# Kernel tuning notes

Hardware: AMD Instinct MI355X
Metric: run time of the kernel (lower is better)

Reference implementation:

```python
import jax, jax.numpy as jnp
import numpy as np
from jax import lax

B, T, D, H = 2048, 512, 8, 80  # batch, seq_len, input_dim, hidden_dim


def setup_inputs() -> dict:
    key = jax.random.key(0)
    ks = jax.random.split(key, 10)
    s = 1.0 / np.sqrt(H)  # torch LSTM init: U(-1/sqrt(H), 1/sqrt(H))
    u = lambda k, shape: jax.random.uniform(k, shape, jnp.float32, -s, s)
    return {
        "X": jax.random.normal(ks[0], (B, T, D), jnp.float32),
        "W_ih0": u(ks[1], (4 * H, D)),
        "W_hh0": u(ks[2], (4 * H, H)),
        "b_ih0": u(ks[3], (4 * H,)),
        "b_hh0": u(ks[4], (4 * H,)),
        "W_ih1": u(ks[5], (4 * H, H)),
        "W_hh1": u(ks[6], (4 * H, H)),
        "b_ih1": u(ks[7], (4 * H,)),
        "b_hh1": u(ks[8], (4 * H,)),
        "X_seq_len": jax.random.randint(ks[9], (B,), 1, T + 1),  # valid lengths in [1, T]
    }


def _lstm_layer(x_tm, W_ih, W_hh, b_ih, b_hh):
    """x_tm: [T, B, Din] time-major. Returns hidden states [T, B, H].
    PyTorch gate order: i, f, g, o."""
    # Precompute all input projections in one big GEMM: [T, B, 4H]
    xg = jnp.einsum('tbd,gd->tbg', x_tm, W_ih) + b_ih + b_hh
    Hd = W_hh.shape[1]
    h0 = jnp.zeros((x_tm.shape[1], Hd), x_tm.dtype)

    def step(carry, g_in):
        h, c = carry
        g = g_in + h @ W_hh.T  # [B, 4H]
        i, f, gg, o = jnp.split(g, 4, axis=-1)
        c = jax.nn.sigmoid(f) * c + jax.nn.sigmoid(i) * jnp.tanh(gg)
        h = jax.nn.sigmoid(o) * jnp.tanh(c)
        return (h, c), h

    _, hs = lax.scan(step, (h0, h0), xg)
    return hs


def reference(X, W_ih0, W_hh0, b_ih0, b_hh0, W_ih1, W_hh1, b_ih1, b_hh1, X_seq_len):
    x = jnp.swapaxes(X, 0, 1)  # [T, B, D] time-major for scan
    h1 = _lstm_layer(x, W_ih0, W_hh0, b_ih0, b_hh0)   # [T, B, H]
    h2 = _lstm_layer(h1, W_ih1, W_hh1, b_ih1, b_hh1)  # [T, B, H]
    # Gather last valid timestep per sequence (packed-seq semantics):
    # state at t = len-1 only depends on inputs <= len-1, so padded run is equivalent.
    idx = X_seq_len - 1
    out = h2[idx, jnp.arange(X.shape[0])]  # [B, H]
    return out
```

## Files before the change

### kernel.cpp

```cpp
#include <hip/hip_runtime.h>
#include <math.h>

#define B_   2048
#define T_   512
#define D_   8
#define H_   80
#define NB   16
#define NBLK (B_ / NB)
#define NTH  640
#define KS0  3
#define KS1  5
#define A0S  256
#define A1S  384
#define A0BUF (16 * A0S)
#define A1BUF (16 * A1S)
#define LOG2E 1.44269504f
#define K2    2.88539008f

typedef float f32x4  __attribute__((ext_vector_type(4)));
typedef short bf16x8 __attribute__((ext_vector_type(8)));
typedef unsigned short u16x4 __attribute__((ext_vector_type(4)));

__device__ __forceinline__ float E2(float x) {
#if __has_builtin(__builtin_amdgcn_exp2f)
  return __builtin_amdgcn_exp2f(x);
#else
  return __expf(x * 0.6931471806f);
#endif
}
__device__ __forceinline__ unsigned short f2bf(float f) {
  unsigned u = __builtin_bit_cast(unsigned, f);
  return (unsigned short)((u + 0x7FFFu + ((u >> 16) & 1u)) >> 16);
}
__device__ __forceinline__ float bf2f(unsigned short b) {
  unsigned u = ((unsigned)b) << 16;
  return __builtin_bit_cast(float, u);
}
__device__ __forceinline__ int swz(int row, int byte_in_row) {
  return byte_in_row ^ ((row & 7) << 4);
}
__device__ __forceinline__ float cell(float ai, float af, float ag, float ao,
                                      float& c) {
  const float ei = E2(-ai), ef = E2(-af), eg = E2(-ag), eo = E2(-ao);
  const float P  = (1.0f + ei) * (1.0f + eg);
  const float pf = 1.0f + ef;
  const float cn = __builtin_fmaf(c, P, (1.0f - eg) * pf)
                 * __builtin_amdgcn_rcpf(P * pf);
  c = cn;
  const float ec = E2(-K2 * fabsf(cn));
  const float t  = (1.0f - ec)
                 * __builtin_amdgcn_rcpf((1.0f + eo) * (1.0f + ec));
  return copysignf(t, cn);
}

__global__ __launch_bounds__(512)
void sort_by_len(const int* __restrict__ slen, int* __restrict__ perm) {
  __shared__ int cnt[513];
  const int tid = threadIdx.x;
  for (int i = tid; i < 513; i += 512) cnt[i] = 0;
  __syncthreads();
  for (int b = tid; b < B_; b += 512) atomicAdd(&cnt[T_ - slen[b]], 1);
  __syncthreads();
  if (tid == 0) { int s = 0;
    for (int k = 0; k < 513; ++k) { int c = cnt[k]; cnt[k] = s; s += c; } }
  __syncthreads();
  for (int b = tid; b < B_; b += 512) {
    int pos = atomicAdd(&cnt[T_ - slen[b]], 1);
    perm[pos] = b;
  }
}

__global__ __launch_bounds__(NTH)
void lstm2_mfma(const float* __restrict__ X,
                const float* __restrict__ Wih0, const float* __restrict__ Whh0,
                const float* __restrict__ bih0, const float* __restrict__ bhh0,
                const float* __restrict__ Wih1, const float* __restrict__ Whh1,
                const float* __restrict__ bih1, const float* __restrict__ bhh1,
                const int* __restrict__ slen, const int* __restrict__ perm,
                float* __restrict__ out)
{
  __shared__ char a0lds[2 * A0BUF];
  __shared__ char a1lds[2 * A1BUF];
  __shared__ int  pbs[NB];
  __shared__ int  lns[NB];

  const int tid = threadIdx.x;
  const int w   = tid >> 6;
  const int l   = tid & 63;
  const int lr  = l & 15;
  const int q   = l >> 4;
  const int L   = (w < 5) ? 0 : 1;
  const int v   = w - 5 * L;
  const int u   = 16 * v + lr;
  const int ub4 = 16 * v + 4 * q;

  if (tid < NB) {
    int pb = perm[blockIdx.x * NB + tid];
    pbs[tid] = pb;
    lns[tid] = slen[pb];
  }

  bf16x8 wf[4][KS1];
  float  bias[4][4];
  if (L == 0) {
    #pragma unroll
    for (int g = 0; g < 4; ++g) {
      const float sc = (g == 2) ? K2 : LOG2E;
      const int n = 80 * g + u;
      #pragma unroll
      for (int r = 0; r < 4; ++r) {
        const int nb = 80 * g + ub4 + r;
        bias[g][r] = (bih0[nb] + bhh0[nb]) * sc;
      }
      #pragma unroll
      for (int ks = 0; ks < KS0; ++ks) {
        bf16x8 vv;
        #pragma unroll
        for (int j = 0; j < 8; ++j) {
          int k = 32 * ks + 8 * q + j;
          float f = (k < 8)  ? Wih0[n * D_ + k]
                  : (k < 16) ? Wih0[n * D_ + (k - 8)]
                             : Whh0[n * H_ + (k - 16)];
          vv[j] = (short)f2bf(f * sc);
        }
        wf[g][ks] = vv;
      }
    }
  } else {
    #pragma unroll
    for (int g = 0; g < 4; ++g) {
      const float sc = (g == 2) ? K2 : LOG2E;
      const int n = 80 * g + u;
      #pragma unroll
      for (int r = 0; r < 4; ++r) {
        const int nb = 80 * g + ub4 + r;
        bias[g][r] = (bih1[nb] + bhh1[nb]) * sc;
      }
      #pragma unroll
      for (int ks = 0; ks < KS1; ++ks) {
        bf16x8 vv;
        #pragma unroll
        for (int j = 0; j < 8; ++j) {
          int k = 32 * ks + 8 * q + j;
          float f = (k < 80) ? Wih1[n * H_ + k] : Whh1[n * H_ + (k - 80)];
          vv[j] = (short)f2bf(f * sc);
        }
        wf[g][ks] = vv;
      }
    }
  }

  for (int i = tid; i < (2 * A0BUF) / 4; i += NTH) ((int*)a0lds)[i] = 0;
  for (int i = tid; i < (2 * A1BUF) / 4; i += NTH) ((int*)a1lds)[i] = 0;
  __syncthreads();

  const int mlen  = lns[0];
  const int pbseq = pbs[lr];
  const int lm1   = lns[lr] - 1;

  const int xs = tid >> 4, xt = (tid & 15) >> 1, xh = tid & 1;
  const float* xbase = nullptr;
  f32x4 xa = {}, xb = {};
  if (tid < 256) {
    xbase = X + (size_t)pbs[xs] * (T_ * D_) + 4 * xh;
    int t0 = xt;     if (t0 > T_ - 1) t0 = T_ - 1;
    int t1 = 8 + xt; if (t1 > T_ - 1) t1 = T_ - 1;
    xa = *(const f32x4*)(xbase + t0 * D_);
    xb = *(const f32x4*)(xbase + t1 * D_);
  }
  #pragma unroll
  for (int tt = 0; tt < 2; ++tt) {
    if (tid < 256 && xt == tt) {
      u16x4 hi, lo;
      #pragma unroll
      for (int j = 0; j < 4; ++j) { hi[j] = f2bf(xa[j]); lo[j] = f2bf(xa[j] - bf2f(hi[j])); }
      char* buf = a0lds + tt * A0BUF;
      *(u16x4*)(buf + xs * A0S + swz(xs, 8 * xh))      = hi;
      *(u16x4*)(buf + xs * A0S + swz(xs, 16 + 8 * xh)) = lo;
    }
  }
  __syncthreads();

  float c[4] = {0.f, 0.f, 0.f, 0.f};

  if (L == 0) {
    f32x4 acc[4] = {};
    #pragma unroll
    for (int ks = 0; ks < KS0; ++ks) {
      bf16x8 a = *(const bf16x8*)(a0lds + lr * A0S + swz(lr, 64 * ks + 16 * q));
      #pragma unroll
      for (int g = 0; g < 4; ++g)
        acc[g] = __builtin_amdgcn_mfma_f32_16x16x32_bf16(wf[g][ks], a, acc[g], 0, 0, 0);
    }
    char* A1w = a1lds;
    char* A0w = a0lds + A0BUF;
    u16x4 hv;
    #pragma unroll
    for (int r = 0; r < 4; ++r) {
      float h = cell(acc[0][r] + bias[0][r], acc[1][r] + bias[1][r],
                     acc[2][r] + bias[2][r], acc[3][r] + bias[3][r], c[r]);
      hv[r] = f2bf(h);
    }
    *(u16x4*)(A1w + lr * A1S + swz(lr, 2 * ub4))      = hv;
    *(u16x4*)(A0w + lr * A0S + swz(lr, 32 + 2 * ub4)) = hv;
  }
  __syncthreads();

  #pragma unroll 2
  for (int i = 0; i < mlen; ++i) {
    const int cur = i & 1, nxt = cur ^ 1;

    if (tid < 256 && ((i + 2) & 7) == 0) {
      xa = xb;
      int tc = i + 10 + xt; if (tc > T_ - 1) tc = T_ - 1;
      xb = *(const f32x4*)(xbase + tc * D_);
    }

    f32x4 acc[4] = {};
    if (L == 1) {
      const char* A1p = a1lds + cur * A1BUF;
      #pragma unroll
      for (int ks = 0; ks < KS1; ++ks) {
        bf16x8 a = *(const bf16x8*)(A1p + lr * A1S + swz(lr, 64 * ks + 16 * q));
        #pragma unroll
        for (int g = 0; g < 4; ++g)
          acc[g] = __builtin_amdgcn_mfma_f32_16x16x32_bf16(wf[g][ks], a, acc[g], 0, 0, 0);
      }
    } else {
      const char* A0p = a0lds + nxt * A0BUF;
      #pragma unroll
      for (int ks = 0; ks < KS0; ++ks) {
        bf16x8 a = *(const bf16x8*)(A0p + lr * A0S + swz(lr, 64 * ks + 16 * q));
        #pragma unroll
        for (int g = 0; g < 4; ++g)
          acc[g] = __builtin_amdgcn_mfma_f32_16x16x32_bf16(wf[g][ks], a, acc[g], 0, 0, 0);
      }
    }

    if (tid < 256 && xt == ((i + 2) & 7)) {
      u16x4 hi, lo;
      #pragma unroll
      for (int j = 0; j < 4; ++j) { hi[j] = f2bf(xa[j]); lo[j] = f2bf(xa[j] - bf2f(hi[j])); }
      char* buf = a0lds + cur * A0BUF;
      *(u16x4*)(buf + xs * A0S + swz(xs, 8 * xh))      = hi;
      *(u16x4*)(buf + xs * A0S + swz(xs, 16 + 8 * xh)) = lo;
    }

    char* A1n = a1lds + nxt * A1BUF;
    char* A0c = a0lds + cur * A0BUF;

    if (L == 1) {
      float h[4];
      u16x4 hv;
      #pragma unroll
      for (int r = 0; r < 4; ++r) {
        h[r] = cell(acc[0][r] + bias[0][r], acc[1][r] + bias[1][r],
                    acc[2][r] + bias[2][r], acc[3][r] + bias[3][r], c[r]);
        hv[r] = f2bf(h[r]);
      }
      *(u16x4*)(A1n + lr * A1S + swz(lr, 160 + 2 * ub4)) = hv;
      if (i == lm1)
        *(f32x4*)(out + (size_t)pbseq * H_ + ub4) = (f32x4){h[0], h[1], h[2], h[3]};
    } else {
      u16x4 hv;
      #pragma unroll
      for (int r = 0; r < 4; ++r) {
        float h = cell(acc[0][r] + bias[0][r], acc[1][r] + bias[1][r],
                       acc[2][r] + bias[2][r], acc[3][r] + bias[3][r], c[r]);
        hv[r] = f2bf(h);
      }
      *(u16x4*)(A1n + lr * A1S + swz(lr, 2 * ub4))      = hv;
      *(u16x4*)(A0c + lr * A0S + swz(lr, 32 + 2 * ub4)) = hv;
    }
    __syncthreads();
  }
}

extern "C" void kernel_launch(void* const* d_in, const int* in_sizes, int n_in,
                              void* d_out, int out_size, void* d_ws, size_t ws_size,
                              hipStream_t stream) {
  const float* X    = (const float*)d_in[0];
  const float* Wih0 = (const float*)d_in[1];
  const float* Whh0 = (const float*)d_in[2];
  const float* bih0 = (const float*)d_in[3];
  const float* bhh0 = (const float*)d_in[4];
  const float* Wih1 = (const float*)d_in[5];
  const float* Whh1 = (const float*)d_in[6];
  const float* bih1 = (const float*)d_in[7];
  const float* bhh1 = (const float*)d_in[8];
  const int*   slen = (const int*)d_in[9];
  int* perm = (int*)d_ws;

  sort_by_len<<<1, 512, 0, stream>>>(slen, perm);
  lstm2_mfma<<<NBLK, NTH, 0, stream>>>(
      X, Wih0, Whh0, bih0, bhh0, Wih1, Whh1, bih1, bhh1, slen, perm,
      (float*)d_out);
}
```

Measured before the change: 598.7 us.

## Split LSTM layers into producer/consumer blocks linked by a global-memory ring

Layer 0 and layer 1 of each 16-sequence group now run in two separate 320-thread blocks instead of one 640-thread block. Layer 0 publishes its hidden states into a 16-slot global ring buffer and a progress flag. Layer 1 spins on that flag and prefetches the next step's input from the ring, so each block syncs only its own five waves per step and the two layers can drift up to eight steps apart. The cost is global-memory traffic and atomic polling between blocks, and the scheme deadlocks unless both blocks of a pair are resident at the same time.

New measurement: 1.165 ms. 1.95x slower.

```diff
diff --git a/kernel.cpp b/kernel.cpp
--- a/kernel.cpp
+++ b/kernel.cpp
@@ -6,20 +6,23 @@
 #define D_   8
 #define H_   80
 #define NB   16
-#define NBLK (B_ / NB)
-#define NTH  640
+#define NPAIR (B_ / NB)
+#define NTH  320
 #define KS0  3
 #define KS1  5
 #define A0S  256
 #define A1S  384
 #define A0BUF (16 * A0S)
 #define A1BUF (16 * A1S)
+#define RING_D 16
+#define RSLOT  2560
 #define LOG2E 1.44269504f
 #define K2    2.88539008f
 
 typedef float f32x4  __attribute__((ext_vector_type(4)));
 typedef short bf16x8 __attribute__((ext_vector_type(8)));
 typedef unsigned short u16x4 __attribute__((ext_vector_type(4)));
+typedef unsigned long long u64;
 
 __device__ __forceinline__ float E2(float x) {
 #if __has_builtin(__builtin_amdgcn_exp2f)
@@ -54,9 +57,11 @@
 }
 
 __global__ __launch_bounds__(512)
-void sort_by_len(const int* __restrict__ slen, int* __restrict__ perm) {
+void sort_by_len(const int* __restrict__ slen, int* __restrict__ perm,
+                 int* __restrict__ flags) {
   __shared__ int cnt[513];
   const int tid = threadIdx.x;
+  if (tid < 256) flags[tid] = 0;
   for (int i = tid; i < 513; i += 512) cnt[i] = 0;
   __syncthreads();
   for (int b = tid; b < B_; b += 512) atomicAdd(&cnt[T_ - slen[b]], 1);
@@ -71,38 +76,41 @@
 }
 
 __global__ __launch_bounds__(NTH)
-void lstm2_mfma(const float* __restrict__ X,
-                const float* __restrict__ Wih0, const float* __restrict__ Whh0,
-                const float* __restrict__ bih0, const float* __restrict__ bhh0,
-                const float* __restrict__ Wih1, const float* __restrict__ Whh1,
-                const float* __restrict__ bih1, const float* __restrict__ bhh1,
-                const int* __restrict__ slen, const int* __restrict__ perm,
-                float* __restrict__ out)
+void lstm2_pc(const float* __restrict__ X,
+              const float* __restrict__ Wih0, const float* __restrict__ Whh0,
+              const float* __restrict__ bih0, const float* __restrict__ bhh0,
+              const float* __restrict__ Wih1, const float* __restrict__ Whh1,
+              const float* __restrict__ bih1, const float* __restrict__ bhh1,
+              const int* __restrict__ slen, const int* __restrict__ perm,
+              int* __restrict__ prog0, int* __restrict__ prog1,
+              char* __restrict__ ring, float* __restrict__ out)
 {
-  __shared__ char a0lds[2 * A0BUF];
-  __shared__ char a1lds[2 * A1BUF];
-  __shared__ int  pbs[NB];
-  __shared__ int  lns[NB];
+  __shared__ char lds[2 * A1BUF];
+  __shared__ int  pbs[NB], lns[NB];
 
   const int tid = threadIdx.x;
   const int w   = tid >> 6;
   const int l   = tid & 63;
   const int lr  = l & 15;
   const int q   = l >> 4;
-  const int L   = (w < 5) ? 0 : 1;
-  const int v   = w - 5 * L;
-  const int u   = 16 * v + lr;
-  const int ub4 = 16 * v + 4 * q;
+  const int u   = 16 * w + lr;
+  const int ub4 = 16 * w + 4 * q;
+  const int p   = blockIdx.x >> 1;
+  const int role = blockIdx.x & 1;
+
+  int* prog0p = prog0 + p;
+  int* prog1p = prog1 + p;
+  char* ringp = ring + (size_t)p * (RING_D * RSLOT);
 
   if (tid < NB) {
-    int pb = perm[blockIdx.x * NB + tid];
+    int pb = perm[p * NB + tid];
     pbs[tid] = pb;
     lns[tid] = slen[pb];
   }
 
-  bf16x8 wf[4][KS1];
-  float  bias[4][4];
-  if (L == 0) {
+  if (role == 0) {
+    bf16x8 wf[4][KS0];
+    float  bias[4][4];
     #pragma unroll
     for (int g = 0; g < 4; ++g) {
       const float sc = (g == 2) ? K2 : LOG2E;
@@ -126,7 +134,92 @@
         wf[g][ks] = vv;
       }
     }
+    for (int i = tid; i < (2 * A0BUF) / 4; i += NTH) ((int*)lds)[i] = 0;
+    __syncthreads();
+    const int mlen = lns[0];
+
+    const int xs = tid >> 4, xt = (tid & 15) >> 1, xh = tid & 1;
+    const float* xbase = nullptr;
+    f32x4 xa = {}, xb = {};
+    if (tid < 256) {
+      xbase = X + (size_t)pbs[xs] * (T_ * D_) + 4 * xh;
+      int t0 = xt;     if (t0 > T_ - 1) t0 = T_ - 1;
+      int t1 = 8 + xt; if (t1 > T_ - 1) t1 = T_ - 1;
+      xa = *(const f32x4*)(xbase + t0 * D_);
+      xb = *(const f32x4*)(xbase + t1 * D_);
+    }
+    if (tid < 256 && xt == 0) {
+      u16x4 hi, lo;
+      #pragma unroll
+      for (int j = 0; j < 4; ++j) { hi[j] = f2bf(xa[j]); lo[j] = f2bf(xa[j] - bf2f(hi[j])); }
+      *(u16x4*)(lds + xs * A0S + swz(xs, 8 * xh))      = hi;
+      *(u16x4*)(lds + xs * A0S + swz(xs, 16 + 8 * xh)) = lo;
+    }
+    __syncthreads();
+
+    float c[4] = {0.f, 0.f, 0.f, 0.f};
+    int p1c = 0;
+
+    #pragma unroll 2
+    for (int i = 0; i < mlen; ++i) {
+      if (tid == 0)
+        __hip_atomic_store(prog0p, i, __ATOMIC_RELEASE, __HIP_MEMORY_SCOPE_AGENT);
+      if ((i & 7) == 0 && i >= 16) {
+        const int target = i - 8;
+        if (p1c < target) {
+          int pv;
+          do {
+            pv = __hip_atomic_load(prog1p, __ATOMIC_ACQUIRE, __HIP_MEMORY_SCOPE_AGENT);
+            if (pv < target) __builtin_amdgcn_s_sleep(4);
+          } while (pv < target);
+          p1c = pv;
+        }
+      }
+      if (tid < 256 && ((i + 1) & 7) == 0) {
+        xa = xb;
+        int tc = i + 9 + xt; if (tc > T_ - 1) tc = T_ - 1;
+        xb = *(const f32x4*)(xbase + tc * D_);
+      }
+
+      const char* A0p = lds + (i & 1) * A0BUF;
+      f32x4 acc[4] = {};
+      #pragma unroll
+      for (int ks = 0; ks < KS0; ++ks) {
+        bf16x8 a = *(const bf16x8*)(A0p + lr * A0S + swz(lr, 64 * ks + 16 * q));
+        #pragma unroll
+        for (int g = 0; g < 4; ++g)
+          acc[g] = __builtin_amdgcn_mfma_f32_16x16x32_bf16(wf[g][ks], a, acc[g], 0, 0, 0);
+      }
+
+      char* A0n = lds + ((i + 1) & 1) * A0BUF;
+      if (tid < 256 && xt == ((i + 1) & 7)) {
+        u16x4 hi, lo;
+        #pragma unroll
+        for (int j = 0; j < 4; ++j) { hi[j] = f2bf(xa[j]); lo[j] = f2bf(xa[j] - bf2f(hi[j])); }
+        *(u16x4*)(A0n + xs * A0S + swz(xs, 8 * xh))      = hi;
+        *(u16x4*)(A0n + xs * A0S + swz(xs, 16 + 8 * xh)) = lo;
+      }
+
+      u16x4 hv;
+      #pragma unroll
+      for (int r = 0; r < 4; ++r) {
+        float h = cell(acc[0][r] + bias[0][r], acc[1][r] + bias[1][r],
+                       acc[2][r] + bias[2][r], acc[3][r] + bias[3][r], c[r]);
+        hv[r] = f2bf(h);
+      }
+      *(u16x4*)(A0n + lr * A0S + swz(lr, 32 + 2 * ub4)) = hv;
+      __hip_atomic_store((u64*)(ringp + (size_t)(i & (RING_D - 1)) * RSLOT
+                                + lr * 160 + 2 * ub4),
+                         __builtin_bit_cast(u64, hv),
+                         __ATOMIC_RELAXED, __HIP_MEMORY_SCOPE_AGENT);
+      __syncthreads();
+    }
+    if (tid == 0)
+      __hip_atomic_store(prog0p, mlen, __ATOMIC_RELEASE, __HIP_MEMORY_SCOPE_AGENT);
+
   } else {
+    bf16x8 wf[4][KS1];
+    float  bias[4][4];
     #pragma unroll
     for (int g = 0; g < 4; ++g) {
       const float sc = (g == 2) ? K2 : LOG2E;
@@ -148,77 +241,56 @@
         wf[g][ks] = vv;
       }
     }
-  }
-
-  for (int i = tid; i < (2 * A0BUF) / 4; i += NTH) ((int*)a0lds)[i] = 0;
-  for (int i = tid; i < (2 * A1BUF) / 4; i += NTH) ((int*)a1lds)[i] = 0;
-  __syncthreads();
-
-  const int mlen  = lns[0];
-  const int pbseq = pbs[lr];
-  const int lm1   = lns[lr] - 1;
-
-  const int xs = tid >> 4, xt = (tid & 15) >> 1, xh = tid & 1;
-  const float* xbase = nullptr;
-  f32x4 xa = {}, xb = {};
-  if (tid < 256) {
-    xbase = X + (size_t)pbs[xs] * (T_ * D_) + 4 * xh;
-    int t0 = xt;     if (t0 > T_ - 1) t0 = T_ - 1;
-    int t1 = 8 + xt; if (t1 > T_ - 1) t1 = T_ - 1;
-    xa = *(const f32x4*)(xbase + t0 * D_);
-    xb = *(const f32x4*)(xbase + t1 * D_);
-  }
-  #pragma unroll
-  for (int tt = 0; tt < 2; ++tt) {
-    if (tid < 256 && xt == tt) {
-      u16x4 hi, lo;
-      #pragma unroll
-      for (int j = 0; j < 4; ++j) { hi[j] = f2bf(xa[j]); lo[j] = f2bf(xa[j] - bf2f(hi[j])); }
-      char* buf = a0lds + tt * A0BUF;
-      *(u16x4*)(buf + xs * A0S + swz(xs, 8 * xh))      = hi;
-      *(u16x4*)(buf + xs * A0S + swz(xs, 16 + 8 * xh)) = lo;
-    }
-  }
-  __syncthreads();
-
-  float c[4] = {0.f, 0.f, 0.f, 0.f};
-
-  if (L == 0) {
-    f32x4 acc[4] = {};
-    #pragma unroll
-    for (int ks = 0; ks < KS0; ++ks) {
-      bf16x8 a = *(const bf16x8*)(a0lds + lr * A0S + swz(lr, 64 * ks + 16 * q));
-      #pragma unroll
-      for (int g = 0; g < 4; ++g)
-        acc[g] = __builtin_amdgcn_mfma_f32_16x16x32_bf16(wf[g][ks], a, acc[g], 0, 0, 0);
-    }
-    char* A1w = a1lds;
-    char* A0w = a0lds + A0BUF;
-    u16x4 hv;
-    #pragma unroll
-    for (int r = 0; r < 4; ++r) {
-      float h = cell(acc[0][r] + bias[0][r], acc[1][r] + bias[1][r],
-                     acc[2][r] + bias[2][r], acc[3][r] + bias[3][r], c[r]);
-      hv[r] = f2bf(h);
-    }
-    *(u16x4*)(A1w + lr * A1S + swz(lr, 2 * ub4))      = hv;
-    *(u16x4*)(A0w + lr * A0S + swz(lr, 32 + 2 * ub4)) = hv;
-  }
-  __syncthreads();
-
-  #pragma unroll 2
-  for (int i = 0; i < mlen; ++i) {
-    const int cur = i & 1, nxt = cur ^ 1;
-
-    if (tid < 256 && ((i + 2) & 7) == 0) {
-      xa = xb;
-      int tc = i + 10 + xt; if (tc > T_ - 1) tc = T_ - 1;
-      xb = *(const f32x4*)(xbase + tc * D_);
-    }
-
-    f32x4 acc[4] = {};
-    if (L == 1) {
-      const char* A1p = a1lds + cur * A1BUF;
+    for (int i = tid; i < (2 * A1BUF) / 4; i += NTH) ((int*)lds)[i] = 0;
+    __syncthreads();
+    const int mlen  = lns[0];
+    const int pbseq = pbs[lr];
+    const int lm1   = lns[lr] - 1;
+
+    const int ss = tid / 20, qd = tid - (tid / 20) * 20;
+    int p0c = 0;
+    {
+      const int target = (mlen < 5) ? mlen : 5;
+      int pv;
+      do {
+        pv = __hip_atomic_load(prog0p, __ATOMIC_ACQUIRE, __HIP_MEMORY_SCOPE_AGENT);
+        if (pv < target) __builtin_amdgcn_s_sleep(4);
+      } while (pv < target);
+      p0c = pv;
+    }
+    {
+      u64 v0 = __hip_atomic_load((const u64*)(ringp + ss * 160 + qd * 8),
+                                 __ATOMIC_RELAXED, __HIP_MEMORY_SCOPE_AGENT);
+      *(u64*)(lds + ss * A1S + swz(ss, qd * 8)) = v0;
+    }
+    __syncthreads();
+
+    float c[4] = {0.f, 0.f, 0.f, 0.f};
+
+    #pragma unroll 2
+    for (int i = 0; i < mlen; ++i) {
+      if ((i & 3) == 0) {
+        if (tid == 0)
+          __hip_atomic_store(prog1p, i, __ATOMIC_RELAXED, __HIP_MEMORY_SCOPE_AGENT);
+        int target = i + 5; if (target > mlen) target = mlen;
+        if (p0c < target) {
+          int pv;
+          do {
+            pv = __hip_atomic_load(prog0p, __ATOMIC_ACQUIRE, __HIP_MEMORY_SCOPE_AGENT);
+            if (pv < target) __builtin_amdgcn_s_sleep(4);
+          } while (pv < target);
+          p0c = pv;
+        }
+      }
+      const bool pf = (i + 1 < mlen);
+      u64 vst = 0;
+      if (pf)
+        vst = __hip_atomic_load((const u64*)(ringp
+                + (size_t)((i + 1) & (RING_D - 1)) * RSLOT + ss * 160 + qd * 8),
+                __ATOMIC_RELAXED, __HIP_MEMORY_SCOPE_AGENT);
+
+      const char* A1p = lds + (i & 1) * A1BUF;
+      f32x4 acc[4] = {};
       #pragma unroll
       for (int ks = 0; ks < KS1; ++ks) {
         bf16x8 a = *(const bf16x8*)(A1p + lr * A1S + swz(lr, 64 * ks + 16 * q));
@@ -226,30 +298,8 @@
         for (int g = 0; g < 4; ++g)
           acc[g] = __builtin_amdgcn_mfma_f32_16x16x32_bf16(wf[g][ks], a, acc[g], 0, 0, 0);
       }
-    } else {
-      const char* A0p = a0lds + nxt * A0BUF;
-      #pragma unroll
-      for (int ks = 0; ks < KS0; ++ks) {
-        bf16x8 a = *(const bf16x8*)(A0p + lr * A0S + swz(lr, 64 * ks + 16 * q));
-        #pragma unroll
-        for (int g = 0; g < 4; ++g)
-          acc[g] = __builtin_amdgcn_mfma_f32_16x16x32_bf16(wf[g][ks], a, acc[g], 0, 0, 0);
-      }
-    }
-
-    if (tid < 256 && xt == ((i + 2) & 7)) {
-      u16x4 hi, lo;
-      #pragma unroll
-      for (int j = 0; j < 4; ++j) { hi[j] = f2bf(xa[j]); lo[j] = f2bf(xa[j] - bf2f(hi[j])); }
-      char* buf = a0lds + cur * A0BUF;
-      *(u16x4*)(buf + xs * A0S + swz(xs, 8 * xh))      = hi;
-      *(u16x4*)(buf + xs * A0S + swz(xs, 16 + 8 * xh)) = lo;
-    }
-
-    char* A1n = a1lds + nxt * A1BUF;
-    char* A0c = a0lds + cur * A0BUF;
-
-    if (L == 1) {
+
+      char* A1n = lds + ((i + 1) & 1) * A1BUF;
       float h[4];
       u16x4 hv;
       #pragma unroll
@@ -259,20 +309,14 @@
         hv[r] = f2bf(h[r]);
       }
       *(u16x4*)(A1n + lr * A1S + swz(lr, 160 + 2 * ub4)) = hv;
+      if (pf)
+        *(u64*)(A1n + ss * A1S + swz(ss, qd * 8)) = vst;
       if (i == lm1)
         *(f32x4*)(out + (size_t)pbseq * H_ + ub4) = (f32x4){h[0], h[1], h[2], h[3]};
-    } else {
-      u16x4 hv;
-      #pragma unroll
-      for (int r = 0; r < 4; ++r) {
-        float h = cell(acc[0][r] + bias[0][r], acc[1][r] + bias[1][r],
-                       acc[2][r] + bias[2][r], acc[3][r] + bias[3][r], c[r]);
-        hv[r] = f2bf(h);
-      }
-      *(u16x4*)(A1n + lr * A1S + swz(lr, 2 * ub4))      = hv;
-      *(u16x4*)(A0c + lr * A0S + swz(lr, 32 + 2 * ub4)) = hv;
-    }
-    __syncthreads();
+      __syncthreads();
+    }
+    if (tid == 0)
+      __hip_atomic_store(prog1p, mlen, __ATOMIC_RELAXED, __HIP_MEMORY_SCOPE_AGENT);
   }
 }
 
@@ -289,10 +333,15 @@
   const float* bih1 = (const float*)d_in[7];
   const float* bhh1 = (const float*)d_in[8];
   const int*   slen = (const int*)d_in[9];
-  int* perm = (int*)d_ws;
-
-  sort_by_len<<<1, 512, 0, stream>>>(slen, perm);
-  lstm2_mfma<<<NBLK, NTH, 0, stream>>>(
+
+  int*  perm  = (int*)d_ws;
+  int*  flags = (int*)((char*)d_ws + 8192);
+  int*  prog0 = flags;
+  int*  prog1 = flags + 128;
+  char* ring  = (char*)d_ws + 16384;
+
+  sort_by_len<<<1, 512, 0, stream>>>(slen, perm, flags);
+  lstm2_pc<<<2 * NPAIR, NTH, 0, stream>>>(
       X, Wih0, Whh0, bih0, bhh0, Wih1, Whh1, bih1, bhh1, slen, perm,
-      (float*)d_out);
-}
+      prog0, prog1, ring, (float*)d_out);
+}
```
